# Optimization experiments

Hardware: AMD Instinct MI355X
Metric: run time of the kernel (lower is better)

Reference implementation:

```python
import jax, jax.numpy as jnp
import numpy as np

N_NODES = 50000
N_EDGES = 800000
NNIN = 128
NOPEN = 64
NLAYER = 8
NUM_OUT = 40
H = 0.1  # integration step h


def setup_inputs() -> dict:
    key = jax.random.key(0)
    k1, k2, k3, k4, k5, k6 = jax.random.split(key, 6)
    xn = jax.random.normal(k1, (1, NNIN, N_NODES), dtype=jnp.float32)
    I = jax.random.randint(k2, (N_EDGES,), 0, N_NODES)
    J = jax.random.randint(k3, (N_EDGES,), 0, N_NODES)
    K1Nopen = jax.random.normal(k4, (NOPEN, NNIN), dtype=jnp.float32) * 0.01
    # identityInit: square per-layer kernels near identity
    eye = jnp.eye(NOPEN, dtype=jnp.float32)
    KN2 = eye[None, :, :] + jax.random.normal(k5, (NLAYER, NOPEN, NOPEN), dtype=jnp.float32) * 0.01
    KNclose = jax.random.normal(k6, (NUM_OUT, NOPEN), dtype=jnp.float32) * 0.01
    return {"xn": xn, "I": I, "J": J, "n_nodes": N_NODES,
            "K1Nopen": K1Nopen, "KN2": KN2, "KNclose": KNclose}


def gcn_norm(I, J, n_nodes):
    # PyG gcn_norm with self-loops: w = D^-1/2 A_hat D^-1/2 (deg over col index)
    loop = jnp.arange(n_nodes)
    I2 = jnp.concatenate([I, loop])
    J2 = jnp.concatenate([J, loop])
    w = jnp.ones(I2.shape[0], dtype=jnp.float32)
    deg = jax.ops.segment_sum(w, J2, num_segments=n_nodes)
    dinv = jnp.where(deg > 0, 1.0 / jnp.sqrt(deg), 0.0)
    W = dinv[I2] * w * dinv[J2]
    return I2, J2, W


def reference(xn, I, J, n_nodes, K1Nopen, KN2, KNclose):
    I2, J2, W = gcn_norm(I, J, n_nodes)
    We = W[None, None, :]  # broadcast over [batch, channel, edge]

    # opening 1x1 conv + relu (K1Nopen non-square branch of singleLayer)
    xn = jax.nn.relu(jnp.einsum('oc,bcn->bon', K1Nopen, xn))
    xn_old = xn

    def step(carry, K):
        xn, xn_old = carry
        # nodeGrad: gather + weighted difference -> [1, C, E]
        g = We * (xn[:, :, I2] - xn[:, :, J2])
        # square singleLayer (relu=False): conv(K) -> tanh -> conv(K.T)
        t = jnp.tanh(jnp.einsum('oc,bce->boe', K, g))
        d = jnp.einsum('co,boe->bce', K, t)
        # edgeDiv: weighted scatter-add back to nodes
        dW = We * d
        dxn = jnp.zeros_like(xn).at[:, :, I2].add(dW).at[:, :, J2].add(-dW)
        # leapfrog wave integration
        xn_new = 2.0 * xn - xn_old - (H * H) * dxn
        return (xn_new, xn), None

    (xn, xn_old), _ = jax.lax.scan(step, (xn, xn_old), KN2)

    # closing 1x1 conv, then squeeze().t() -> [n_nodes, num_output]
    out = jnp.einsum('oc,bcn->bon', KNclose, xn)
    return out[0].T
```

## Files before the change

### kernel.cpp

```cpp
#include <hip/hip_runtime.h>
#include <hip/hip_bf16.h>
#include <hip/hip_fp16.h>

#define N_NODES 50000
#define N_EDGES 800000
#define NNIN    128
#define NOPEN   64
#define NUM_OUT 40
#define NLAYER  8
#define HSQ     0.01f

#define NDIG  ((N_NODES + 255) >> 8)
#define EPB   2048
#define P1B   ((N_EDGES + EPB - 1) / EPB)
#define P2CAP 9216
#define SBIN  32

typedef float f32x2 __attribute__((ext_vector_type(2)));

__device__ __forceinline__ f32x2 pk_fma(f32x2 a, f32x2 b, f32x2 c) {
    f32x2 d;
    asm("v_pk_fma_f32 %0, %1, %2, %3" : "=v"(d) : "v"(a), "v"(b), "v"(c));
    return d;
}
__device__ __forceinline__ f32x2 pk_mul(f32x2 a, f32x2 b) {
    f32x2 d;
    asm("v_pk_mul_f32 %0, %1, %2" : "=v"(d) : "v"(a), "v"(b));
    return d;
}
__device__ __forceinline__ f32x2 h2f(__half2 h) {
    float2 f = __half22float2(h);
    return (f32x2){f.x, f.y};
}


__global__ void deg_init(int* __restrict__ degi) {
    int n = blockIdx.x * 256 + threadIdx.x;
    if (n < N_NODES) degi[n] = 1;
}

__global__ __launch_bounds__(256) void count_all(const int* __restrict__ I,
                                                 const int* __restrict__ J,
                                                 int* __restrict__ degi,
                                                 int* __restrict__ bh) {
    __shared__ int h[NDIG];
    int t = threadIdx.x, b = blockIdx.x;
    for (int i = t; i < NDIG; i += 256) h[i] = 0;
    __syncthreads();
    int e0 = b * EPB;
    int e1 = min(e0 + EPB, N_EDGES);
    for (int e = e0 + t; e < e1; e += 256) {
        int i = I[e], j = J[e];
        atomicAdd(&degi[j], 1);
        atomicAdd(&h[i >> 8], 1);
        atomicAdd(&h[j >> 8], 1);
    }
    __syncthreads();
    for (int i = t; i < NDIG; i += 256) bh[b * NDIG + i] = h[i];
}

__global__ void calc_dinv(const int* __restrict__ degi, float* __restrict__ dinv) {
    int n = blockIdx.x * 256 + threadIdx.x;
    if (n < N_NODES) dinv[n] = rsqrtf((float)degi[n]);
}

__global__ __launch_bounds__(512) void col_scan(const int* __restrict__ bh,
                                                int* __restrict__ off,
                                                int* __restrict__ total) {
    __shared__ int sh[512];
    int d = blockIdx.x, t = threadIdx.x;
    int v = (t < P1B) ? bh[t * NDIG + d] : 0;
    sh[t] = v;
    __syncthreads();
#pragma unroll
    for (int o = 1; o < 512; o <<= 1) {
        int x = (t >= o) ? sh[t - o] : 0;
        __syncthreads();
        sh[t] += x;
        __syncthreads();
    }
    if (t < P1B) off[d * P1B + t] = sh[t] - v;
    if (t == 511) total[d] = sh[511];
}

__global__ __launch_bounds__(256) void dig_scan(const int* __restrict__ total,
                                                int* __restrict__ dig_raw,
                                                int* __restrict__ dig_pad) {
    __shared__ int sh[256], sh2[256];
    int t = threadIdx.x;
    int v   = (t < NDIG) ? total[t] : 0;
    int cap = (t < NDIG) ? ((v + 256 * 7 + 7) & ~7) : 0;
    sh[t] = v; sh2[t] = cap;
    __syncthreads();
#pragma unroll
    for (int o = 1; o < 256; o <<= 1) {
        int x = (t >= o) ? sh[t - o] : 0;
        int y = (t >= o) ? sh2[t - o] : 0;
        __syncthreads();
        sh[t] += x; sh2[t] += y;
        __syncthreads();
    }
    if (t < NDIG) { dig_raw[t] = sh[t] - v; dig_pad[t] = sh2[t] - cap; }
}

__global__ __launch_bounds__(256) void pass1_scatter(const int* __restrict__ I,
                                                     const int* __restrict__ J,
                                                     const int* __restrict__ off,
                                                     const int* __restrict__ dig_raw,
                                                     unsigned* __restrict__ ebuf) {
    __shared__ int cnt2[NDIG];
    __shared__ int base[NDIG];
    int t = threadIdx.x, b = blockIdx.x;
    for (int i = t; i < NDIG; i += 256) {
        cnt2[i] = 0;
        base[i] = dig_raw[i] + off[i * P1B + b];
    }
    __syncthreads();
    int e0 = b * EPB;
    int e1 = min(e0 + EPB, N_EDGES);
    for (int e = e0 + t; e < e1; e += 256) {
        int i = I[e], j = J[e];
        int li = atomicAdd(&cnt2[i >> 8], 1);
        ebuf[base[i >> 8] + li] = ((unsigned)i << 16) | (unsigned)j;
        int lj = atomicAdd(&cnt2[j >> 8], 1);
        ebuf[base[j >> 8] + lj] = ((unsigned)j << 16) | (unsigned)i;
    }
}

__global__ __launch_bounds__(256) void pass2_csr(const unsigned* __restrict__ ebuf,
                                                 const int* __restrict__ dig_raw,
                                                 const int* __restrict__ total,
                                                 const int* __restrict__ dig_pad,
                                                 const float* __restrict__ dinv,
                                                 int* __restrict__ row_start,
                                                 int* __restrict__ deg2,
                                                 int2* __restrict__ ent) {
    __shared__ unsigned eb[P2CAP];
    __shared__ int cnt[256], loc[256], cur[256];
    int d = blockIdx.x, t = threadIdx.x;
    int s = dig_raw[d];
    int c = total[d]; if (c > P2CAP) c = P2CAP;
    for (int i = t; i < c; i += 256) eb[i] = ebuf[s + i];
    cnt[t] = 0;
    __syncthreads();
    for (int i = t; i < c; i += 256)
        atomicAdd(&cnt[(eb[i] >> 16) & 255], 1);
    __syncthreads();
    int pc = (cnt[t] + 7) & ~7;
    loc[t] = pc;
    __syncthreads();
#pragma unroll
    for (int o = 1; o < 256; o <<= 1) {
        int x = (t >= o) ? loc[t - o] : 0;
        __syncthreads();
        loc[t] += x;
        __syncthreads();
    }
    int mybase = dig_pad[d] + loc[t] - pc;
    int n = (d << 8) + t;
    if (n < N_NODES) {
        row_start[n] = mybase;
        deg2[n] = cnt[t];
    }
    cur[t] = mybase;
    __syncthreads();
    for (int i = t; i < c; i += 256) {
        unsigned v = eb[i];
        int ln = (int)(v >> 16) & 255;
        int other = (int)(v & 0xffffu);
        int p = atomicAdd(&cur[ln], 1);
        float w = dinv[(d << 8) + ln] * dinv[other];
        ent[p] = make_int2(other, __float_as_int(w));
    }
    __syncthreads();
    if (n < N_NODES) {
        for (int p = mybase + cnt[t]; p < mybase + pc; p++)
            ent[p] = make_int2(n, 0);
    }
}

__global__ __launch_bounds__(256) void sort_hist(const int* __restrict__ deg2,
                                                 int* __restrict__ sbh) {
    __shared__ int h[SBIN];
    int t = threadIdx.x, b = blockIdx.x;
    if (t < SBIN) h[t] = 0;
    __syncthreads();
    int n = b * 256 + t;
    if (n < N_NODES) atomicAdd(&h[min(deg2[n], 255) >> 3], 1);
    __syncthreads();
    if (t < SBIN) sbh[b * SBIN + t] = h[t];
}

__global__ __launch_bounds__(256) void sort_scan(const int* __restrict__ sbh,
                                                 int* __restrict__ soff,
                                                 int* __restrict__ stot) {
    __shared__ int sh[256];
    int bin = blockIdx.x, t = threadIdx.x;
    int v = (t < NDIG) ? sbh[t * SBIN + bin] : 0;
    sh[t] = v;
    __syncthreads();
#pragma unroll
    for (int o = 1; o < 256; o <<= 1) {
        int x = (t >= o) ? sh[t - o] : 0;
        __syncthreads();
        sh[t] += x;
        __syncthreads();
    }
    if (t < NDIG) soff[bin * NDIG + t] = sh[t] - v;
    if (t == 255) stot[bin] = sh[255];
}

__global__ void sort_base(const int* __restrict__ stot, int* __restrict__ sbase) {
    int t = threadIdx.x;
    if (t < SBIN) {
        int acc = 0;
        for (int b2 = t + 1; b2 < SBIN; b2++) acc += stot[b2];
        sbase[t] = acc;
    }
}

__global__ __launch_bounds__(256) void sort_scatter(const int* __restrict__ deg2,
                                                    const int* __restrict__ soff,
                                                    const int* __restrict__ sbase,
                                                    int* __restrict__ perm) {
    __shared__ int c[SBIN];
    __shared__ int bb[SBIN];
    int t = threadIdx.x, b = blockIdx.x;
    if (t < SBIN) { c[t] = 0; bb[t] = sbase[t] + soff[t * NDIG + b]; }
    __syncthreads();
    int n = b * 256 + t;
    if (n < N_NODES) {
        int bin = min(deg2[n], 255) >> 3;
        int p = atomicAdd(&c[bin], 1);
        perm[bb[bin] + p] = n;
    }
}

__global__ __launch_bounds__(256) void first_layer(const float* __restrict__ xn,
                                                   const float* __restrict__ k1f,
                                                   float* __restrict__ x_cur,
                                                   float* __restrict__ x_old) {
    __shared__ float Ks[NOPEN * 129];
    __shared__ float xs[32 * 64];
    int t = threadIdx.x;
    int n0 = blockIdx.x * 64;
    for (int idx = t; idx < NOPEN * NNIN; idx += 256)
        Ks[(idx >> 7) * 129 + (idx & 127)] = k1f[idx];

    int tn = t & 15, to = t >> 4;
    float acc[4][4] = {};
    for (int c0 = 0; c0 < NNIN; c0 += 32) {
        __syncthreads();
        for (int idx = t; idx < 32 * 64; idx += 256) {
            int ci = idx >> 6, n = idx & 63;
            int gn = n0 + n;
            xs[ci * 64 + n] = (gn < N_NODES) ? xn[(size_t)(c0 + ci) * N_NODES + gn] : 0.f;
        }
        __syncthreads();
        for (int ci = 0; ci < 32; ci++) {
            float xv[4], kv[4];
#pragma unroll
            for (int i2 = 0; i2 < 4; i2++) xv[i2] = xs[ci * 64 + tn * 4 + i2];
#pragma unroll
            for (int j = 0; j < 4; j++) kv[j] = Ks[(to * 4 + j) * 129 + c0 + ci];
#pragma unroll
            for (int i2 = 0; i2 < 4; i2++)
#pragma unroll
                for (int j = 0; j < 4; j++) acc[i2][j] += xv[i2] * kv[j];
        }
    }
#pragma unroll
    for (int i2 = 0; i2 < 4; i2++) {
        int node = n0 + tn * 4 + i2;
        if (node < N_NODES) {
            float4 st;
            st.x = fmaxf(acc[i2][0], 0.f);
            st.y = fmaxf(acc[i2][1], 0.f);
            st.z = fmaxf(acc[i2][2], 0.f);
            st.w = fmaxf(acc[i2][3], 0.f);
            *(float4*)&x_cur[(size_t)node * 64 + to * 4] = st;
            *(float4*)&x_old[(size_t)node * 64 + to * 4] = st;
        }
    }
}

__global__ __launch_bounds__(256) void mat_y(const float* __restrict__ x,
                                             const float* __restrict__ K,
                                             __half* __restrict__ Y) {
    __shared__ float Ks[64 * 65];
    __shared__ float xs[64 * 65];
    int t = threadIdx.x, n0 = blockIdx.x * 64;
    for (int idx = t; idx < 4096; idx += 256) {
        int r = idx >> 6, c = idx & 63;
        Ks[r * 65 + c] = K[idx];
        int gn = n0 + r;
        xs[r * 65 + c] = (gn < N_NODES) ? x[(size_t)gn * 64 + c] : 0.f;
    }
    __syncthreads();
    int tn = t & 15, to = t >> 4;
    float acc[4][4] = {};
    for (int c = 0; c < 64; c++) {
        float xv[4], kv[4];
#pragma unroll
        for (int i2 = 0; i2 < 4; i2++) xv[i2] = xs[(tn * 4 + i2) * 65 + c];
#pragma unroll
        for (int j = 0; j < 4; j++) kv[j] = Ks[(to * 4 + j) * 65 + c];
#pragma unroll
        for (int i2 = 0; i2 < 4; i2++)
#pragma unroll
            for (int j = 0; j < 4; j++) acc[i2][j] += xv[i2] * kv[j];
    }
#pragma unroll
    for (int i2 = 0; i2 < 4; i2++) {
        int node = n0 + tn * 4 + i2;
        if (node < N_NODES) {
            __half2 h0 = __floats2half2_rn(acc[i2][0], acc[i2][1]);
            __half2 h1 = __floats2half2_rn(acc[i2][2], acc[i2][3]);
            __half2* dst = (__half2*)&Y[(size_t)node * 64 + to * 4];
            dst[0] = h0;
            dst[1] = h1;
        }
    }
}

__global__ __launch_bounds__(512) void gather_update(const __half* __restrict__ Y,
                                                     const float* __restrict__ x_cur,
                                                     const float* __restrict__ x_old,
                                                     const int2* __restrict__ ent,
                                                     const int* __restrict__ row_start,
                                                     const int* __restrict__ deg2,
                                                     const int* __restrict__ perm,
                                                     const float* __restrict__ K,
                                                     const float* __restrict__ Kn,
                                                     float* __restrict__ x_out,
                                                     __half* __restrict__ Y_out) {
    __shared__ float Ks[64 * 66];
    __shared__ float Ksn[64 * 66];
    __shared__ float Ss[8][64];
    int t = threadIdx.x;
    int wv = t >> 6, lane = t & 63;
    int c2  = lane & 31;
    int sel = lane >> 5;
    int n = __builtin_amdgcn_readfirstlane(perm[blockIdx.x * 8 + wv]);

    int beg = row_start[n];
    int dg  = deg2[n];
    f32x2 yn = h2f(*(const __half2*)&Y[((size_t)n << 6) + 2 * c2]);
    float xc = x_cur[(size_t)n * 64 + lane];
    float xo = x_old[(size_t)n * 64 + lane];

    for (int idx = t; idx < 4096; idx += 512) {
        int r = idx >> 6, cc = idx & 63;
        Ks[r * 66 + cc]  = K[idx];
        Ksn[r * 66 + cc] = Kn[idx];
    }
    __syncthreads();

    beg = __builtin_amdgcn_readfirstlane(beg);
    dg  = __builtin_amdgcn_readfirstlane(dg);
    int end = beg + ((dg + 7) & ~7);

    const f32x2 C3v  = {-0.33333334f,  -0.33333334f };
    const f32x2 C5v  = { 0.13333334f,   0.13333334f };
    const f32x2 C7v  = {-0.053968254f, -0.053968254f};
    const f32x2 ONEv = { 1.0f, 1.0f };
    const f32x2 NEG1 = {-1.0f, -1.0f};

    const __half2* Yc2 = (const __half2*)Y;
    int sel4 = sel << 2;

    int4 A0, B0, A1, B1;
    __half2 G0, G1, G2, G3;
    int k = beg;
    if (k < end) {
        A0 = *(const int4*)(ent + k + sel4);
        B0 = *(const int4*)(ent + k + sel4 + 2);
    }
    if (k + 8 < end) {
        A1 = *(const int4*)(ent + k + 8 + sel4);
        B1 = *(const int4*)(ent + k + 8 + sel4 + 2);
    }
    if (k < end) {
        G0 = Yc2[((unsigned)A0.x << 5) + c2];
        G1 = Yc2[((unsigned)A0.z << 5) + c2];
        G2 = Yc2[((unsigned)B0.x << 5) + c2];
        G3 = Yc2[((unsigned)B0.z << 5) + c2];
    }

    f32x2 s = {0.f, 0.f};
#define EDGE_ACC(gh, wbits)                                                 \
        {                                                                   \
            float wf = __int_as_float(wbits);                               \
            f32x2 wvv = {wf, wf};                                           \
            f32x2 dd  = pk_fma(h2f(gh), NEG1, yn);                          \
            f32x2 zz  = pk_mul(wvv, dd);                                    \
            f32x2 z2  = pk_mul(zz, zz);                                     \
            f32x2 pp  = pk_fma(z2, pk_fma(z2, pk_fma(z2, C7v, C5v), C3v), ONEv); \
            s = pk_fma(pk_mul(wvv, zz), pp, s);                             \
        }
    for (; k < end; k += 8) {
        int4 A2, B2;
        if (k + 16 < end) {
            A2 = *(const int4*)(ent + k + 16 + sel4);
            B2 = *(const int4*)(ent + k + 16 + sel4 + 2);
        }
        __half2 P0, P1, P2, P3;
        if (k + 8 < end) {
            P0 = Yc2[((unsigned)A1.x << 5) + c2];
            P1 = Yc2[((unsigned)A1.z << 5) + c2];
            P2 = Yc2[((unsigned)B1.x << 5) + c2];
            P3 = Yc2[((unsigned)B1.z << 5) + c2];
        }
        EDGE_ACC(G0, A0.y)
        EDGE_ACC(G1, A0.w)
        EDGE_ACC(G2, B0.y)
        EDGE_ACC(G3, B0.w)
        A0 = A1; B0 = B1; A1 = A2; B1 = B2;
        G0 = P0; G1 = P1; G2 = P2; G3 = P3;
    }
#undef EDGE_ACC

    s.x += __shfl_xor(s.x, 32, 64);
    s.y += __shfl_xor(s.y, 32, 64);
    if (lane < 32) *(f32x2*)&Ss[wv][2 * c2] = s;

    f32x2 acc2 = {0.f, 0.f};
#pragma unroll
    for (int o = 0; o < 64; o += 2)
        acc2 = pk_fma(*(const f32x2*)&Ks[lane * 66 + o],
                      *(const f32x2*)&Ss[wv][o], acc2);
    float xnew = 2.f * xc - xo - HSQ * (acc2.x + acc2.y);
    __builtin_nontemporal_store(xnew, &x_out[(size_t)n * 64 + lane]);
    Ss[wv][lane] = xnew;
    f32x2 acc3 = {0.f, 0.f};
#pragma unroll
    for (int c = 0; c < 64; c += 2)
        acc3 = pk_fma(*(const f32x2*)&Ksn[lane * 66 + c],
                      *(const f32x2*)&Ss[wv][c], acc3);
    Y_out[((size_t)n << 6) + lane] = __float2half(acc3.x + acc3.y);
}

__global__ __launch_bounds__(256) void out_kernel(const float* __restrict__ x,
                                                  const float* __restrict__ Kc,
                                                  float* __restrict__ out) {
    __shared__ float xs[64 * 65];
    __shared__ float Ks[40 * 65];
    int t = threadIdx.x, n0 = blockIdx.x * 64;
    for (int idx = t; idx < 4096; idx += 256) {
        int r = idx >> 6, c = idx & 63;
        int gn = n0 + r;
        xs[r * 65 + c] = (gn < N_NODES) ? x[(size_t)gn * 64 + c] : 0.f;
    }
    for (int idx = t; idx < NUM_OUT * 64; idx += 256) {
        int r = idx >> 6, c = idx & 63;
        Ks[r * 65 + c] = Kc[idx];
    }
    __syncthreads();
    if (t < 160) {
        int tn = t & 15, to = t >> 4;
        float acc[4][4] = {};
        for (int c = 0; c < 64; c++) {
            float xv[4], kv[4];
#pragma unroll
            for (int i2 = 0; i2 < 4; i2++) xv[i2] = xs[(tn * 4 + i2) * 65 + c];
#pragma unroll
            for (int j = 0; j < 4; j++) kv[j] = Ks[(to * 4 + j) * 65 + c];
#pragma unroll
            for (int i2 = 0; i2 < 4; i2++)
#pragma unroll
                for (int j = 0; j < 4; j++) acc[i2][j] += xv[i2] * kv[j];
        }
#pragma unroll
        for (int i2 = 0; i2 < 4; i2++) {
            int node = n0 + tn * 4 + i2;
            if (node < N_NODES) {
#pragma unroll
                for (int j = 0; j < 4; j++)
                    out[(size_t)node * NUM_OUT + to * 4 + j] = acc[i2][j];
            }
        }
    }
}

extern "C" void kernel_launch(void* const* d_in, const int* in_sizes, int n_in,
                              void* d_out, int out_size, void* d_ws, size_t ws_size,
                              hipStream_t stream) {
    const float* xn = (const float*)d_in[0];
    const int*   I  = (const int*)d_in[1];
    const int*   J  = (const int*)d_in[2];
    const float* K1 = (const float*)d_in[4];
    const float* K2 = (const float*)d_in[5];
    const float* Kc = (const float*)d_in[6];

    const size_t NC = (size_t)N_NODES * NOPEN;
    float*    f       = (float*)d_ws;
    float*    x_cur   = f;
    float*    x_old   = f + NC;
    __half*   Y0      = (__half*)(f + 2 * NC);
    __half*   Y1      = (__half*)(f + 2 * NC + NC / 2);
    float*    dinv    = f + 3 * NC;
    int*      degi    = (int*)(dinv + N_NODES);
    int*      deg2    = degi + N_NODES;
    int*      row_st  = deg2 + N_NODES;
    int*      total   = row_st + N_NODES;
    int*      dig_raw = total + 256;
    int*      dig_pad = dig_raw + 256;
    int*      bh      = dig_pad + 256;
    int*      off     = bh + 80000;
    int*      perm    = off + 80000;
    int*      sbh     = perm + 50048;
    int*      soff    = sbh + 6400;
    int*      stot    = soff + 6400;
    int*      sbase   = stot + 64;
    unsigned* ebuf    = (unsigned*)(sbase + 64);
    int2*     ent     = (int2*)(ebuf + 2 * (size_t)N_EDGES);

    dim3 B(256);
    const int GN = (N_NODES + 255) / 256;

    deg_init<<<GN, B, 0, stream>>>(degi);
    count_all<<<P1B, B, 0, stream>>>(I, J, degi, bh);
    calc_dinv<<<GN, B, 0, stream>>>(degi, dinv);
    col_scan<<<NDIG, dim3(512), 0, stream>>>(bh, off, total);
    dig_scan<<<1, B, 0, stream>>>(total, dig_raw, dig_pad);
    pass1_scatter<<<P1B, B, 0, stream>>>(I, J, off, dig_raw, ebuf);
    pass2_csr<<<NDIG, B, 0, stream>>>(ebuf, dig_raw, total, dig_pad, dinv, row_st, deg2, ent);

    sort_hist<<<NDIG, B, 0, stream>>>(deg2, sbh);
    sort_scan<<<SBIN, B, 0, stream>>>(sbh, soff, stot);
    sort_base<<<1, dim3(64), 0, stream>>>(stot, sbase);
    sort_scatter<<<NDIG, B, 0, stream>>>(deg2, soff, sbase, perm);

    const int NB = (N_NODES + 63) / 64;
    first_layer<<<NB, B, 0, stream>>>(xn, K1, x_cur, x_old);
    mat_y<<<NB, B, 0, stream>>>(x_cur, K2, Y0);

    __half* Yin = Y0;
    __half* Yout = Y1;
    float* xc = x_cur;
    float* xo = x_old;
    for (int l = 0; l < NLAYER; l++) {
        const float* Kl = K2 + l * NOPEN * NOPEN;
        const float* Knext = K2 + (l + 1 < NLAYER ? l + 1 : l) * NOPEN * NOPEN;
        gather_update<<<N_NODES / 8, dim3(512), 0, stream>>>(
            Yin, xc, xo, ent, row_st, deg2, perm, Kl, Knext, xo, Yout);
        float* tmp = xc; xc = xo; xo = tmp;
        __half* th = Yin; Yin = Yout; Yout = th;
    }
    out_kernel<<<NB, B, 0, stream>>>(xc, Kc, (float*)d_out);
}
```

Measured before the change: 726.4 us.

## Split edge list into 16-bit ids and weights with deep asm-pipelined gather

Edge entries move from interleaved int2 (id, weight) to separate arrays: 16-bit node ids and float weights. This cuts the bytes read per edge in the gather kernel. The gather loop becomes a 4-stage software pipeline built from inline global_load asm and explicit vmcnt waits, keeping more Y gathers in flight. Rows are padded to multiples of 32 edges and launch_bounds gets an occupancy hint. In exchange the padding adds wasted edge work, and ebuf now shares memory with x_cur. The hand-tuned waitcnt counts are fragile.

```diff
diff --git a/kernel.cpp b/kernel.cpp
--- a/kernel.cpp
+++ b/kernel.cpp
@@ -15,8 +15,11 @@
 #define P1B   ((N_EDGES + EPB - 1) / EPB)
 #define P2CAP 9216
 #define SBIN  32
+#define ENT_CAP 3200000
 
 typedef float f32x2 __attribute__((ext_vector_type(2)));
+typedef int   i32x4 __attribute__((ext_vector_type(4)));
+typedef int   i32x2 __attribute__((ext_vector_type(2)));
 
 __device__ __forceinline__ f32x2 pk_fma(f32x2 a, f32x2 b, f32x2 c) {
     f32x2 d;
@@ -32,6 +35,23 @@
     float2 f = __half22float2(h);
     return (f32x2){f.x, f.y};
 }
+__device__ __forceinline__ f32x2 h2fu(unsigned u) {
+    __half2 h = __builtin_bit_cast(__half2, u);
+    float2 f = __half22float2(h);
+    return (f32x2){f.x, f.y};
+}
+
+__device__ __forceinline__ void gload4(i32x4 &d, unsigned vo, const void* b) {
+    asm volatile("global_load_dwordx4 %0, %1, %2" : "=v"(d) : "v"(vo), "s"(b));
+}
+__device__ __forceinline__ void gload2(i32x2 &d, unsigned vo, const void* b) {
+    asm volatile("global_load_dwordx2 %0, %1, %2" : "=v"(d) : "v"(vo), "s"(b));
+}
+__device__ __forceinline__ void gload1(unsigned &d, unsigned vo, const void* b) {
+    asm volatile("global_load_dword %0, %1, %2" : "=v"(d) : "v"(vo), "s"(b));
+}
+#define WAITCNT(n) do { asm volatile("s_waitcnt vmcnt(" #n ")"); \
+                        __builtin_amdgcn_sched_barrier(0); } while (0)
 
 
 __global__ void deg_init(int* __restrict__ degi) {
@@ -89,7 +109,7 @@
     __shared__ int sh[256], sh2[256];
     int t = threadIdx.x;
     int v   = (t < NDIG) ? total[t] : 0;
-    int cap = (t < NDIG) ? ((v + 256 * 7 + 7) & ~7) : 0;
+    int cap = (t < NDIG) ? ((v + 256 * 31 + 7) & ~7) : 0;
     sh[t] = v; sh2[t] = cap;
     __syncthreads();
 #pragma unroll
@@ -134,7 +154,8 @@
                                                  const float* __restrict__ dinv,
                                                  int* __restrict__ row_start,
                                                  int* __restrict__ deg2,
-                                                 int2* __restrict__ ent) {
+                                                 unsigned short* __restrict__ eid,
+                                                 float* __restrict__ ewt) {
     __shared__ unsigned eb[P2CAP];
     __shared__ int cnt[256], loc[256], cur[256];
     int d = blockIdx.x, t = threadIdx.x;
@@ -146,7 +167,9 @@
     for (int i = t; i < c; i += 256)
         atomicAdd(&cnt[(eb[i] >> 16) & 255], 1);
     __syncthreads();
-    int pc = (cnt[t] + 7) & ~7;
+    int ch = (cnt[t] + 7) >> 3;
+    ch = (ch + 3) & ~3;
+    int pc = ch << 3;
     loc[t] = pc;
     __syncthreads();
 #pragma unroll
@@ -169,13 +192,15 @@
         int ln = (int)(v >> 16) & 255;
         int other = (int)(v & 0xffffu);
         int p = atomicAdd(&cur[ln], 1);
-        float w = dinv[(d << 8) + ln] * dinv[other];
-        ent[p] = make_int2(other, __float_as_int(w));
+        eid[p] = (unsigned short)other;
+        ewt[p] = dinv[(d << 8) + ln] * dinv[other];
     }
     __syncthreads();
     if (n < N_NODES) {
-        for (int p = mybase + cnt[t]; p < mybase + pc; p++)
-            ent[p] = make_int2(n, 0);
+        for (int p = mybase + cnt[t]; p < mybase + pc; p++) {
+            eid[p] = (unsigned short)n;
+            ewt[p] = 0.f;
+        }
     }
 }
 
@@ -323,17 +348,19 @@
     }
 }
 
-__global__ __launch_bounds__(512) void gather_update(const __half* __restrict__ Y,
-                                                     const float* __restrict__ x_cur,
-                                                     const float* __restrict__ x_old,
-                                                     const int2* __restrict__ ent,
-                                                     const int* __restrict__ row_start,
-                                                     const int* __restrict__ deg2,
-                                                     const int* __restrict__ perm,
-                                                     const float* __restrict__ K,
-                                                     const float* __restrict__ Kn,
-                                                     float* __restrict__ x_out,
-                                                     __half* __restrict__ Y_out) {
+__global__ __launch_bounds__(512, 6) void gather_update(
+        const __half* __restrict__ Y,
+        const float* __restrict__ x_cur,
+        const float* __restrict__ x_old,
+        const unsigned short* __restrict__ eid,
+        const float* __restrict__ ewt,
+        const int* __restrict__ row_start,
+        const int* __restrict__ deg2,
+        const int* __restrict__ perm,
+        const float* __restrict__ K,
+        const float* __restrict__ Kn,
+        float* __restrict__ x_out,
+        __half* __restrict__ Y_out) {
     __shared__ float Ks[64 * 66];
     __shared__ float Ksn[64 * 66];
     __shared__ float Ss[8][64];
@@ -358,7 +385,8 @@
 
     beg = __builtin_amdgcn_readfirstlane(beg);
     dg  = __builtin_amdgcn_readfirstlane(dg);
-    int end = beg + ((dg + 7) & ~7);
+    int ch = (dg + 7) >> 3;
+    int nch4 = (ch + 3) & ~3;
 
     const f32x2 C3v  = {-0.33333334f,  -0.33333334f };
     const f32x2 C5v  = { 0.13333334f,   0.13333334f };
@@ -366,57 +394,90 @@
     const f32x2 ONEv = { 1.0f, 1.0f };
     const f32x2 NEG1 = {-1.0f, -1.0f};
 
-    const __half2* Yc2 = (const __half2*)Y;
-    int sel4 = sel << 2;
-
-    int4 A0, B0, A1, B1;
-    __half2 G0, G1, G2, G3;
-    int k = beg;
-    if (k < end) {
-        A0 = *(const int4*)(ent + k + sel4);
-        B0 = *(const int4*)(ent + k + sel4 + 2);
-    }
-    if (k + 8 < end) {
-        A1 = *(const int4*)(ent + k + 8 + sel4);
-        B1 = *(const int4*)(ent + k + 8 + sel4 + 2);
-    }
-    if (k < end) {
-        G0 = Yc2[((unsigned)A0.x << 5) + c2];
-        G1 = Yc2[((unsigned)A0.z << 5) + c2];
-        G2 = Yc2[((unsigned)B0.x << 5) + c2];
-        G3 = Yc2[((unsigned)B0.z << 5) + c2];
-    }
-
     f32x2 s = {0.f, 0.f};
-#define EDGE_ACC(gh, wbits)                                                 \
-        {                                                                   \
-            float wf = __int_as_float(wbits);                               \
-            f32x2 wvv = {wf, wf};                                           \
-            f32x2 dd  = pk_fma(h2f(gh), NEG1, yn);                          \
-            f32x2 zz  = pk_mul(wvv, dd);                                    \
-            f32x2 z2  = pk_mul(zz, zz);                                     \
-            f32x2 pp  = pk_fma(z2, pk_fma(z2, pk_fma(z2, C7v, C5v), C3v), ONEv); \
-            s = pk_fma(pk_mul(wvv, zz), pp, s);                             \
-        }
-    for (; k < end; k += 8) {
-        int4 A2, B2;
-        if (k + 16 < end) {
-            A2 = *(const int4*)(ent + k + 16 + sel4);
-            B2 = *(const int4*)(ent + k + 16 + sel4 + 2);
-        }
-        __half2 P0, P1, P2, P3;
-        if (k + 8 < end) {
-            P0 = Yc2[((unsigned)A1.x << 5) + c2];
-            P1 = Yc2[((unsigned)A1.z << 5) + c2];
-            P2 = Yc2[((unsigned)B1.x << 5) + c2];
-            P3 = Yc2[((unsigned)B1.z << 5) + c2];
-        }
-        EDGE_ACC(G0, A0.y)
-        EDGE_ACC(G1, A0.w)
-        EDGE_ACC(G2, B0.y)
-        EDGE_ACC(G3, B0.w)
-        A0 = A1; B0 = B1; A1 = A2; B1 = B2;
-        G0 = P0; G1 = P1; G2 = P2; G3 = P3;
+
+#define EDGE_ACC(gu, wi)                                                    \
+    {                                                                       \
+        float wf = __int_as_float(wi);                                      \
+        f32x2 wvv = {wf, wf};                                               \
+        f32x2 dd  = pk_fma(h2fu(gu), NEG1, yn);                             \
+        f32x2 zz  = pk_mul(wvv, dd);                                        \
+        f32x2 z2  = pk_mul(zz, zz);                                         \
+        f32x2 pp  = pk_fma(z2, pk_fma(z2, pk_fma(z2, C7v, C5v), C3v), ONEv);\
+        s = pk_fma(pk_mul(wvv, zz), pp, s);                                 \
+    }
+
+    if (nch4 > 0) {
+        int lastc = nch4 - 1;
+        int begi = beg * 2;
+        int begw = beg * 4;
+        unsigned seli = (unsigned)(sel << 3);
+        unsigned selw = (unsigned)(sel << 4);
+        unsigned c2b  = (unsigned)(c2 << 2);
+        const void* eidv = (const void*)eid;
+        const void* ewtv = (const void*)ewt;
+        const void* Yv   = (const void*)Y;
+
+        i32x2 Id0, Id1, Id2, Id3;
+        i32x4 W0, W1, W2, W3;
+        unsigned G00, G01, G02, G03, G10, G11, G12, G13;
+        unsigned G20, G21, G22, G23, G30, G31, G32, G33;
+
+        gload2(Id0, (unsigned)(begi)       + seli, eidv);
+        gload4(W0,  (unsigned)(begw)       + selw, ewtv);
+        gload2(Id1, (unsigned)(begi + 16)  + seli, eidv);
+        gload4(W1,  (unsigned)(begw + 32)  + selw, ewtv);
+        gload2(Id2, (unsigned)(begi + 32)  + seli, eidv);
+        gload4(W2,  (unsigned)(begw + 64)  + selw, ewtv);
+        WAITCNT(4);
+        {
+            unsigned u0 = (unsigned)Id0.x, u1 = (unsigned)Id0.y;
+            gload1(G00, ((u0 & 0xffffu) << 7) + c2b, Yv);
+            gload1(G01, ((u0 >> 16)     << 7) + c2b, Yv);
+            gload1(G02, ((u1 & 0xffffu) << 7) + c2b, Yv);
+            gload1(G03, ((u1 >> 16)     << 7) + c2b, Yv);
+        }
+        gload2(Id3, (unsigned)(begi + 48)  + seli, eidv);
+        gload4(W3,  (unsigned)(begw + 96)  + selw, ewtv);
+        WAITCNT(8);
+        {
+            unsigned u0 = (unsigned)Id1.x, u1 = (unsigned)Id1.y;
+            gload1(G10, ((u0 & 0xffffu) << 7) + c2b, Yv);
+            gload1(G11, ((u0 >> 16)     << 7) + c2b, Yv);
+            gload1(G12, ((u1 & 0xffffu) << 7) + c2b, Yv);
+            gload1(G13, ((u1 >> 16)     << 7) + c2b, Yv);
+        }
+
+#define STAGE(sa, sb)                                                        \
+        {                                                                    \
+            WAITCNT(6);                       \
+            EDGE_ACC(G##sa##0, W##sa.x)                                      \
+            EDGE_ACC(G##sa##1, W##sa.y)                                      \
+            EDGE_ACC(G##sa##2, W##sa.z)                                      \
+            EDGE_ACC(G##sa##3, W##sa.w)                                      \
+            {                                                                \
+                int kc = min(c + 4, lastc);                                  \
+                gload2(Id##sa, (unsigned)(begi + kc * 16) + seli, eidv);     \
+                gload4(W##sa,  (unsigned)(begw + kc * 32) + selw, ewtv);     \
+                unsigned u0 = (unsigned)Id##sb.x, u1 = (unsigned)Id##sb.y;   \
+                gload1(G##sb##0, ((u0 & 0xffffu) << 7) + c2b, Yv);           \
+                gload1(G##sb##1, ((u0 >> 16)     << 7) + c2b, Yv);           \
+                gload1(G##sb##2, ((u1 & 0xffffu) << 7) + c2b, Yv);           \
+                gload1(G##sb##3, ((u1 >> 16)     << 7) + c2b, Yv);           \
+            }                                                                \
+            c++;                                                             \
+        }
+
+        int c = 0;
+        while (c < nch4) {
+            STAGE(0, 2)
+            STAGE(1, 3)
+            STAGE(2, 0)
+            STAGE(3, 1)
+        }
+#undef STAGE
+        asm volatile("s_waitcnt vmcnt(0)");
+        __builtin_amdgcn_sched_barrier(0);
     }
 #undef EDGE_ACC
 
@@ -505,15 +566,16 @@
     int*      total   = row_st + N_NODES;
     int*      dig_raw = total + 256;
     int*      dig_pad = dig_raw + 256;
-    int*      bh      = dig_pad + 256;
-    int*      off     = bh + 80000;
-    int*      perm    = off + 80000;
+    int*      perm    = dig_pad + 256;
     int*      sbh     = perm + 50048;
     int*      soff    = sbh + 6400;
     int*      stot    = soff + 6400;
     int*      sbase   = stot + 64;
-    unsigned* ebuf    = (unsigned*)(sbase + 64);
-    int2*     ent     = (int2*)(ebuf + 2 * (size_t)N_EDGES);
+    int*      bh      = sbase + 64;
+    int*      off     = bh + 80000;
+    float*    ewt     = (float*)(off + 80000);
+    unsigned short* eid = (unsigned short*)(ewt + ENT_CAP);
+    unsigned* ebuf    = (unsigned*)x_cur;
 
     dim3 B(256);
     const int GN = (N_NODES + 255) / 256;
@@ -524,7 +586,8 @@
     col_scan<<<NDIG, dim3(512), 0, stream>>>(bh, off, total);
     dig_scan<<<1, B, 0, stream>>>(total, dig_raw, dig_pad);
     pass1_scatter<<<P1B, B, 0, stream>>>(I, J, off, dig_raw, ebuf);
-    pass2_csr<<<NDIG, B, 0, stream>>>(ebuf, dig_raw, total, dig_pad, dinv, row_st, deg2, ent);
+    pass2_csr<<<NDIG, B, 0, stream>>>(ebuf, dig_raw, total, dig_pad, dinv,
+                                      row_st, deg2, eid, ewt);
 
     sort_hist<<<NDIG, B, 0, stream>>>(deg2, sbh);
     sort_scan<<<SBIN, B, 0, stream>>>(sbh, soff, stot);
@@ -543,7 +606,7 @@
         const float* Kl = K2 + l * NOPEN * NOPEN;
         const float* Knext = K2 + (l + 1 < NLAYER ? l + 1 : l) * NOPEN * NOPEN;
         gather_update<<<N_NODES / 8, dim3(512), 0, stream>>>(
-            Yin, xc, xo, ent, row_st, deg2, perm, Kl, Knext, xo, Yout);
+            Yin, xc, xo, eid, ewt, row_st, deg2, perm, Kl, Knext, xo, Yout);
         float* tmp = xc; xc = xo; xo = tmp;
         __half* th = Yin; Yin = Yout; Yout = th;
     }
```

New measurement: 744.4 us. +2.5%, slower.
